# Kernel optimization log

Measured on AMD Instinct MI355X. Metric: run time of the kernel, lower is better.

Reference implementation:

```python
import jax, jax.numpy as jnp
import numpy as np

N_NODES = 10000
N_EDGES = 50000
N_GRAPHS = 64
NODE_DIM = 32
EDGE_DIM = 16
HID = 64
EDGE_HID = 128
OUT_DIM = 1
T_STEPS = 3       # message-passing rounds
S2S_STEPS = 6     # Set2Set processing steps


def setup_inputs() -> dict:
    key = jax.random.key(0)
    ks = jax.random.split(key, 24)
    def w(k, shape, scale):
        return (jax.random.normal(k, shape, dtype=jnp.float32) * scale)
    inp = {}
    inp["node_features"] = jax.random.normal(ks[0], (N_NODES, NODE_DIM), dtype=jnp.float32)
    inp["edge_features"] = jax.random.normal(ks[1], (N_EDGES, EDGE_DIM), dtype=jnp.float32)
    inp["edge_index"] = jax.random.randint(ks[2], (2, N_EDGES), 0, N_NODES, dtype=jnp.int32)
    # sorted, fully-covering graph assignment (nodes of each graph are contiguous)
    inp["batch_indices"] = ((jnp.arange(N_NODES) * N_GRAPHS) // N_NODES).astype(jnp.int32)
    # input projection
    inp["W_proj"] = w(ks[3], (NODE_DIM, HID), 1.0 / np.sqrt(NODE_DIM))
    inp["b_proj"] = jnp.zeros((HID,), jnp.float32)
    # edge network MLP: edge_dim -> edge_hid -> hid*hid
    inp["W_e1"] = w(ks[4], (EDGE_DIM, EDGE_HID), 1.0 / np.sqrt(EDGE_DIM))
    inp["b_e1"] = jnp.zeros((EDGE_HID,), jnp.float32)
    inp["W_e2"] = w(ks[5], (EDGE_HID, HID * HID), 0.01)
    inp["b_e2"] = jnp.zeros((HID * HID,), jnp.float32)
    # GRU cell (torch layout: 3*hid rows = r,z,n)
    inp["W_gih"] = w(ks[6], (3 * HID, HID), 1.0 / np.sqrt(HID))
    inp["W_ghh"] = w(ks[7], (3 * HID, HID), 1.0 / np.sqrt(HID))
    inp["b_gih"] = jnp.zeros((3 * HID,), jnp.float32)
    inp["b_ghh"] = jnp.zeros((3 * HID,), jnp.float32)
    # LSTM cell (torch layout: 4*hid rows = i,f,g,o), input 2*hid
    inp["W_lih"] = w(ks[8], (4 * HID, 2 * HID), 1.0 / np.sqrt(HID))
    inp["W_lhh"] = w(ks[9], (4 * HID, HID), 1.0 / np.sqrt(HID))
    inp["b_lih"] = jnp.zeros((4 * HID,), jnp.float32)
    inp["b_lhh"] = jnp.zeros((4 * HID,), jnp.float32)
    # readout MLP: 2*hid -> hid -> out
    inp["W_m1"] = w(ks[10], (2 * HID, HID), 1.0 / np.sqrt(2 * HID))
    inp["b_m1"] = jnp.zeros((HID,), jnp.float32)
    inp["W_m2"] = w(ks[11], (HID, OUT_DIM), 1.0 / np.sqrt(HID))
    inp["b_m2"] = jnp.zeros((OUT_DIM,), jnp.float32)
    return inp


def _scatter_softmax(e, idx, n_seg):
    mx = jax.ops.segment_max(e, idx, num_segments=n_seg)
    ex = jnp.exp(e - mx[idx])
    s = jax.ops.segment_sum(ex, idx, num_segments=n_seg)
    return ex / (s[idx] + 1e-16)


def _mpnn_forward(node_features, edge_features, edge_index, batch_indices,
                  W_proj, b_proj, W_e1, b_e1, W_e2, b_e2,
                  W_gih, W_ghh, b_gih, b_ghh,
                  W_lih, W_lhh, b_lih, b_lhh,
                  W_m1, b_m1, W_m2, b_m2):
    n_nodes = node_features.shape[0]
    dst = edge_index[0]  # receiving node v
    src = edge_index[1]  # sending node w

    # input projection
    h = node_features @ W_proj + b_proj                       # (N, H)

    # edge network: per-edge transformation matrix A(e_vw) (depends only on edge feats)
    A = jax.nn.relu(edge_features @ W_e1 + b_e1) @ W_e2 + b_e2
    A = A.reshape(-1, HID, HID)                               # (E, H, H)

    # T rounds: gather senders, per-edge bmm, scatter-add to receivers, GRU update
    for _ in range(T_STEPS):
        msgs = jnp.einsum('eij,ej->ei', A, h[src])            # (E, H)
        m = jax.ops.segment_sum(msgs, dst, num_segments=n_nodes)
        gx = m @ W_gih.T + b_gih                              # (N, 3H)
        gh = h @ W_ghh.T + b_ghh
        xr, xz, xn = jnp.split(gx, 3, axis=-1)
        hr, hz, hn = jnp.split(gh, 3, axis=-1)
        r = jax.nn.sigmoid(xr + hr)
        z = jax.nn.sigmoid(xz + hz)
        n = jnp.tanh(xn + r * hn)
        h = (1.0 - z) * n + z * h

    # Set2Set readout
    hs = jnp.zeros((N_GRAPHS, HID), h.dtype)
    cs = jnp.zeros((N_GRAPHS, HID), h.dtype)
    rs = jnp.zeros((N_GRAPHS, HID), h.dtype)
    for _ in range(S2S_STEPS):
        q = hs[batch_indices]                                 # (N, H)
        e = jnp.sum(h * q, axis=-1)                           # (N,)
        a = _scatter_softmax(e, batch_indices, N_GRAPHS)
        rs = jax.ops.segment_sum(a[:, None] * h, batch_indices, num_segments=N_GRAPHS)
        x = jnp.concatenate([hs, rs], axis=-1)                # (G, 2H)
        gates = x @ W_lih.T + b_lih + hs @ W_lhh.T + b_lhh    # (G, 4H)
        i, f, g, o = jnp.split(gates, 4, axis=-1)
        cs = jax.nn.sigmoid(f) * cs + jax.nn.sigmoid(i) * jnp.tanh(g)
        hs = jax.nn.sigmoid(o) * jnp.tanh(cs)
    ge = jnp.concatenate([hs, rs], axis=-1)                   # (G, 2H)
    return jax.nn.relu(ge @ W_m1 + b_m1) @ W_m2 + b_m2        # (G, out)


def reference(node_features, edge_features, edge_index, batch_indices,
              W_proj, b_proj, W_e1, b_e1, W_e2, b_e2,
              W_gih, W_ghh, b_gih, b_ghh,
              W_lih, W_lhh, b_lih, b_lhh,
              W_m1, b_m1, W_m2, b_m2):
    return _mpnn_forward(node_features, edge_features, edge_index, batch_indices,
                         W_proj, b_proj, W_e1, b_e1, W_e2, b_e2,
                         W_gih, W_ghh, b_gih, b_ghh,
                         W_lih, W_lhh, b_lih, b_lhh,
                         W_m1, b_m1, W_m2, b_m2)
```

## Files before the change

kernel.cpp:

```cpp
#include <hip/hip_runtime.h>

#define N_NODES   10000
#define N_EDGES   50000
#define N_GRAPHS  64
#define NODE_DIM  32
#define EDGE_DIM  16
#define HID       64
#define EHID      128
#define T_STEPS   3
#define S2S_STEPS 6

typedef _Float16 half_t;
typedef _Float16 f16x8 __attribute__((ext_vector_type(8)));
typedef float    f32x4 __attribute__((ext_vector_type(4)));

__device__ __forceinline__ float sigf(float x){ return 1.0f/(1.0f + expf(-x)); }

__global__ void k_zero(float* p, int n){
  int i = blockIdx.x*256 + threadIdx.x;
  if (i < n) p[i] = 0.0f;
}

__global__ void k_proj(const float* __restrict__ nf, const float* __restrict__ Wp,
                       const float* __restrict__ bp, float* __restrict__ h){
  int idx = blockIdx.x*256 + threadIdx.x;
  if (idx >= N_NODES*HID) return;
  int n = idx >> 6;
  int c = idx & 63;
  float acc = bp[c];
  const float* row = nf + (size_t)n*NODE_DIM;
  for (int j = 0; j < NODE_DIM; ++j)
    acc = fmaf(row[j], Wp[j*HID + c], acc);
  h[idx] = acc;
}

__global__ void k_tw2(const float* __restrict__ W2, float* __restrict__ Mm){
  int idx = blockIdx.x*256 + threadIdx.x;
  if (idx >= 64*8192) return;
  int j = idx >> 13; int o = idx & 8191; int k = o >> 6; int i = o & 63;
  Mm[idx] = W2[(size_t)k*4096 + i*64 + j];
}

__global__ void k_w2bt(const float* __restrict__ W2, half_t* __restrict__ BT){
  int idx = blockIdx.x*256 + threadIdx.x;
  if (idx >= 512*2*64*8) return;
  int j    = idx & 7;
  int lane = (idx >> 3) & 63;
  int tk   = (idx >> 9) & 1;
  int tn   = idx >> 10;
  int k = tk*32 + ((lane >> 4) << 3) + j;
  int o = tn*16 + (lane & 15);
  BT[idx] = (half_t)W2[(size_t)(o >> 6)*4096 + (o & 63)*64 + k];
}

__global__ void k_h2a(const float* __restrict__ h, half_t* __restrict__ AT){
  int idx = blockIdx.x*256 + threadIdx.x;
  if (idx >= 625*2*64*8) return;
  int j    = idx & 7;
  int lane = (idx >> 3) & 63;
  int tk   = (idx >> 9) & 1;
  int tm   = idx >> 10;
  int mrow = tm*16 + (lane & 15);
  int k    = tk*32 + ((lane >> 4) << 3) + j;
  AT[idx] = (half_t)h[(size_t)mrow*64 + k];
}

__global__ void k_twg(const float* __restrict__ Wg, const float* __restrict__ Wh,
                      float* __restrict__ WgT, float* __restrict__ WhT){
  int idx = blockIdx.x*256 + threadIdx.x;
  if (idx >= 192*64) return;
  int row = idx >> 6;
  int j   = idx & 63;
  WgT[j*192 + row] = Wg[(size_t)row*64 + j];
  WhT[j*192 + row] = Wh[(size_t)row*64 + j];
}

__global__ void k_ehid(const float* __restrict__ ef, const float* __restrict__ W1,
                       const float* __restrict__ b1, float* __restrict__ Hid){
  int idx = blockIdx.x*256 + threadIdx.x;
  if (idx >= N_EDGES*EHID) return;
  int e = idx >> 7, c = idx & 127;
  float acc = b1[c];
  const float* er = ef + (size_t)e*EDGE_DIM;
  for (int j = 0; j < EDGE_DIM; ++j)
    acc = fmaf(er[j], W1[j*EHID + c], acc);
  Hid[idx] = fmaxf(acc, 0.0f);
}

__global__ void k_bh(const float* __restrict__ h, const float* __restrict__ be2,
                     float* __restrict__ bh){
  int idx = blockIdx.x*256 + threadIdx.x;
  if (idx >= N_NODES*HID) return;
  int n = idx >> 6, i = idx & 63;
  float acc = 0.0f;
  const float* row = be2 + (size_t)i*64;
  const float* hr  = h + (size_t)n*64;
  for (int j = 0; j < 64; ++j)
    acc = fmaf(row[j], hr[j], acc);
  bh[idx] = acc;
}

__global__ void k_hist(const int* __restrict__ ei, int* __restrict__ deg){
  int e = blockIdx.x*256 + threadIdx.x;
  if (e >= N_EDGES) return;
  atomicAdd(&deg[ei[N_EDGES + e]], 1);
}

__global__ void k_scan(const int* __restrict__ deg, int* __restrict__ rowptr,
                       int* __restrict__ cursor){
  __shared__ int part[256];
  int t = threadIdx.x;
  int base = t*40;
  int s = 0;
  for (int i = 0; i < 40; ++i){
    int idx = base + i;
    if (idx < N_NODES) s += deg[idx];
  }
  part[t] = s;
  __syncthreads();
  for (int off = 1; off < 256; off <<= 1){
    int v = (t >= off) ? part[t - off] : 0;
    __syncthreads();
    part[t] += v;
    __syncthreads();
  }
  int run = (t > 0) ? part[t - 1] : 0;
  for (int i = 0; i < 40; ++i){
    int idx = base + i;
    if (idx < N_NODES){
      rowptr[idx] = run;
      cursor[idx] = run;
      run += deg[idx];
    }
  }
  if (t == 255) rowptr[N_NODES] = run;
}

__global__ void k_scatter(const int* __restrict__ ei, int* __restrict__ cursor,
                          int* __restrict__ csr){
  int e = blockIdx.x*256 + threadIdx.x;
  if (e >= N_EDGES) return;
  int src = ei[N_EDGES + e];
  int pos = atomicAdd(&cursor[src], 1);
  csr[pos] = e;
}

__global__ void k_cgemm_mfma(const half_t* __restrict__ AT,
                             const half_t* __restrict__ BT,
                             half_t* __restrict__ C){
  __shared__ half_t tile[4][16][64];
  int wv   = threadIdx.x >> 6;
  int lane = threadIdx.x & 63;
  int tm = blockIdx.x*4 + wv;
  bool active = (tm < 625);
  if (!active) tm = 624;
  const f16x8* Ab = (const f16x8*)AT + (size_t)tm*128;
  f16x8 a0 = Ab[lane];
  f16x8 a1 = Ab[64 + lane];
  int tn0 = blockIdx.y*4;
  f32x4 acc[4];
  #pragma unroll
  for (int s = 0; s < 4; ++s){ acc[s][0]=0.f; acc[s][1]=0.f; acc[s][2]=0.f; acc[s][3]=0.f; }
  #pragma unroll
  for (int s = 0; s < 4; ++s){
    const f16x8* Bb = (const f16x8*)BT + (size_t)(tn0 + s)*128;
    f16x8 b0 = Bb[lane];
    f16x8 b1 = Bb[64 + lane];
    acc[s] = __builtin_amdgcn_mfma_f32_16x16x32_f16(a0, b0, acc[s], 0, 0, 0);
    acc[s] = __builtin_amdgcn_mfma_f32_16x16x32_f16(a1, b1, acc[s], 0, 0, 0);
  }
  int quad = lane >> 4;
  int colb = lane & 15;
  #pragma unroll
  for (int s = 0; s < 4; ++s)
    #pragma unroll
    for (int r = 0; r < 4; ++r)
      tile[wv][quad*4 + r][s*16 + colb] = (half_t)acc[s][r];
  __syncthreads();
  if (active){
    int row = lane >> 3;
    int c0  = (lane & 7)*8;
    size_t base = (size_t)tm*16*8192 + (size_t)tn0*16;
    f16x8 v0 = *(const f16x8*)&tile[wv][row][c0];
    f16x8 v1 = *(const f16x8*)&tile[wv][row + 8][c0];
    *(f16x8*)&C[base + (size_t)row*8192 + c0]       = v0;
    *(f16x8*)&C[base + (size_t)(row + 8)*8192 + c0] = v1;
  }
}

__global__ void k_cgemm(const float* __restrict__ h, const float* __restrict__ Mm,
                        half_t* __restrict__ C, int lo, int hi){
  __shared__ float hs[16][64];
  int n0 = lo + blockIdx.x*16;
  int o0 = blockIdx.y*256 + threadIdx.x;
  for (int idx = threadIdx.x; idx < 16*64; idx += 256){
    int nn = idx >> 6, j = idx & 63;
    int node = n0 + nn;
    hs[nn][j] = (node < hi) ? h[(size_t)node*64 + j] : 0.0f;
  }
  __syncthreads();
  float acc0[16], acc1[16];
  #pragma unroll
  for (int nn = 0; nn < 16; ++nn){ acc0[nn] = 0.0f; acc1[nn] = 0.0f; }
  for (int j4 = 0; j4 < 16; ++j4){
    const float* M0 = Mm + (size_t)(j4*4)*8192;
    float a0 = M0[o0],            b0 = M0[o0 + 4096];
    float a1 = M0[8192 + o0],     b1 = M0[8192 + o0 + 4096];
    float a2 = M0[2*8192 + o0],   b2 = M0[2*8192 + o0 + 4096];
    float a3 = M0[3*8192 + o0],   b3 = M0[3*8192 + o0 + 4096];
    #pragma unroll
    for (int nn = 0; nn < 16; ++nn){
      float4 hv = *(const float4*)&hs[nn][j4*4];
      acc0[nn] = fmaf(hv.x, a0, acc0[nn]);
      acc1[nn] = fmaf(hv.x, b0, acc1[nn]);
      acc0[nn] = fmaf(hv.y, a1, acc0[nn]);
      acc1[nn] = fmaf(hv.y, b1, acc1[nn]);
      acc0[nn] = fmaf(hv.z, a2, acc0[nn]);
      acc1[nn] = fmaf(hv.z, b2, acc1[nn]);
      acc0[nn] = fmaf(hv.w, a3, acc0[nn]);
      acc1[nn] = fmaf(hv.w, b3, acc1[nn]);
    }
  }
  #pragma unroll
  for (int nn = 0; nn < 16; ++nn){
    int node = n0 + nn;
    if (node < hi){
      half_t* Cr = C + (size_t)(node - lo)*8192;
      Cr[o0]        = (half_t)acc0[nn];
      Cr[o0 + 4096] = (half_t)acc1[nn];
    }
  }
}

__global__ void MPNN_55705725829535_kernel(const int* __restrict__ rowptr,
                                           const int* __restrict__ csr,
                                           const int* __restrict__ ei,
                                           const float* __restrict__ Hid,
                                           const half_t* __restrict__ C,
                                           const float* __restrict__ bh,
                                           float* __restrict__ m, int lo, int hi){
  __shared__ float hidL[4][8][128];
  int wave = threadIdx.x >> 6;
  int lane = threadIdx.x & 63;
  int s = lo + blockIdx.x*4 + wave;
  if (s >= hi) return;
  int beg = rowptr[s];
  int endp = rowptr[s + 1];
  if (beg == endp) return;
  float bhv = bh[(size_t)s*64 + lane];
  const half_t* Cb = C + (size_t)(s - lo)*8192 + lane;
  float (*hl)[128] = hidL[wave];
  for (int gbeg = beg; gbeg < endp; gbeg += 8){
    int gn = endp - gbeg; if (gn > 8) gn = 8;
    int dsts[8];
    int e0 = csr[gbeg];
    #pragma unroll
    for (int j = 0; j < 8; ++j){
      int e = (j < gn) ? csr[gbeg + j] : e0;
      dsts[j] = ei[e];
      hl[j][lane]      = Hid[(size_t)e*128 + lane];
      hl[j][lane + 64] = Hid[(size_t)e*128 + 64 + lane];
    }
    float acc[8];
    #pragma unroll
    for (int j = 0; j < 8; ++j) acc[j] = 0.0f;
    #pragma unroll 4
    for (int k = 0; k < 128; ++k){
      float c = (float)Cb[k*64];
      #pragma unroll
      for (int j = 0; j < 8; ++j)
        acc[j] = fmaf(hl[j][k], c, acc[j]);
    }
    for (int j = 0; j < gn; ++j)
      atomicAdd(&m[(size_t)dsts[j]*64 + lane], acc[j] + bhv);
  }
}

__global__ void k_msg_fb(const int* __restrict__ ei, const float* __restrict__ ef,
                         const float* __restrict__ W1, const float* __restrict__ b1,
                         const float* __restrict__ W2, const float* __restrict__ be2,
                         const float* __restrict__ h, float* __restrict__ m){
  __shared__ float HidL[EHID];
  __shared__ __align__(16) float hsL[HID];
  int e = blockIdx.x;
  int t = threadIdx.x;
  int src = ei[N_EDGES + e];
  int dst = ei[e];
  {
    float a0 = b1[t];
    float a1 = b1[t + 64];
    const float* er = ef + (size_t)e*EDGE_DIM;
    for (int j = 0; j < EDGE_DIM; ++j){
      float ev = er[j];
      a0 = fmaf(ev, W1[j*EHID + t],      a0);
      a1 = fmaf(ev, W1[j*EHID + t + 64], a1);
    }
    HidL[t]      = fmaxf(a0, 0.0f);
    HidL[t + 64] = fmaxf(a1, 0.0f);
    hsL[t] = h[(size_t)src*64 + t];
  }
  __syncthreads();
  float acc = 0.0f;
  for (int k = 0; k < EHID; ++k){
    float s = HidL[k];
    if (s != 0.0f){
      const float* w = W2 + (size_t)k*4096 + t*64;
      float partial = 0.0f;
      for (int j = 0; j < 64; ++j)
        partial = fmaf(hsL[j], w[j], partial);
      acc = fmaf(s, partial, acc);
    }
  }
  {
    const float* w = be2 + (size_t)t*64;
    for (int j = 0; j < 64; ++j)
      acc = fmaf(hsL[j], w[j], acc);
  }
  atomicAdd(&m[(size_t)dst*64 + t], acc);
}

__global__ void k_gru(float* __restrict__ h, const float* __restrict__ m,
                      const float* __restrict__ WgT, const float* __restrict__ WhT,
                      const float* __restrict__ bg, const float* __restrict__ bhb){
  __shared__ float mld[16][64];
  __shared__ float hld[16][64];
  int t  = threadIdx.x;
  int i  = t & 63;
  int wv = t >> 6;
  int n0 = blockIdx.x*16;
  for (int idx = t; idx < 16*64; idx += 256){
    int nn = idx >> 6, j = idx & 63;
    int node = n0 + nn;
    mld[nn][j] = m[(size_t)node*64 + j];
    hld[nn][j] = h[(size_t)node*64 + j];
  }
  __syncthreads();
  float xr[4], xz[4], xn[4], hr[4], hz[4], hn[4];
  #pragma unroll
  for (int c = 0; c < 4; ++c){
    xr[c] = bg[i];  xz[c] = bg[64 + i];  xn[c] = bg[128 + i];
    hr[c] = bhb[i]; hz[c] = bhb[64 + i]; hn[c] = bhb[128 + i];
  }
  for (int j = 0; j < 64; ++j){
    const float* wg = WgT + j*192;
    const float* wh = WhT + j*192;
    float wgr = wg[i], wgz = wg[64 + i], wgn = wg[128 + i];
    float whr = wh[i], whz = wh[64 + i], whn = wh[128 + i];
    #pragma unroll
    for (int c = 0; c < 4; ++c){
      int nn = wv*4 + c;
      float mj = mld[nn][j];
      float hj = hld[nn][j];
      xr[c] = fmaf(mj, wgr, xr[c]);
      xz[c] = fmaf(mj, wgz, xz[c]);
      xn[c] = fmaf(mj, wgn, xn[c]);
      hr[c] = fmaf(hj, whr, hr[c]);
      hz[c] = fmaf(hj, whz, hz[c]);
      hn[c] = fmaf(hj, whn, hn[c]);
    }
  }
  #pragma unroll
  for (int c = 0; c < 4; ++c){
    int nn = wv*4 + c;
    float r  = sigf(xr[c] + hr[c]);
    float z  = sigf(xz[c] + hz[c]);
    float nv = tanhf(xn[c] + r*hn[c]);
    h[(size_t)(n0 + nn)*64 + i] = (1.0f - z)*nv + z*hld[nn][i];
  }
}

__global__ void k_s2s(const float* __restrict__ h,
                      const float* __restrict__ Wli, const float* __restrict__ Wlh,
                      const float* __restrict__ bli, const float* __restrict__ blh,
                      const float* __restrict__ Wm1, const float* __restrict__ bm1,
                      const float* __restrict__ Wm2, const float* __restrict__ bm2,
                      float* __restrict__ out){
  __shared__ float hc[157*65];
  __shared__ float ea[160];
  __shared__ float x[192];
  __shared__ float gpart[512];
  __shared__ float rsp[8][64];
  __shared__ float wredA[8];
  __shared__ float wredB[8];
  __shared__ float hsb[64];
  __shared__ float csb[64];
  __shared__ float rsb[64];
  int g = blockIdx.x;
  int t = threadIdx.x;
  int lane = t & 63;
  int wv   = t >> 6;
  int start = (g*N_NODES + 63) >> 6;
  int end   = ((g + 1)*N_NODES + 63) >> 6;
  int cnt = end - start;
  const float* hg = h + (size_t)start*64;
  for (int idx = t; idx < cnt*64; idx += 512)
    hc[(idx >> 6)*65 + (idx & 63)] = hg[idx];
  if (t < 64){ hsb[t] = 0.0f; csb[t] = 0.0f; rsb[t] = 0.0f; }
  __syncthreads();
  for (int step = 0; step < S2S_STEPS; ++step){
    float ev = -1e30f;
    if (t < cnt){
      float a = 0.0f;
      const float* hr = &hc[t*65];
      for (int i = 0; i < 64; ++i) a = fmaf(hr[i], hsb[i], a);
      ev = a;
    }
    float v = ev;
    for (int o = 32; o > 0; o >>= 1) v = fmaxf(v, __shfl_xor(v, o));
    if (lane == 0) wredA[wv] = v;
    __syncthreads();
    float mx = wredA[0];
    #pragma unroll
    for (int i = 1; i < 8; ++i) mx = fmaxf(mx, wredA[i]);
    float ex = (t < cnt) ? expf(ev - mx) : 0.0f;
    float sv = ex;
    for (int o = 32; o > 0; o >>= 1) sv += __shfl_xor(sv, o);
    if (lane == 0) wredB[wv] = sv;
    __syncthreads();
    float ssum = 0.0f;
    #pragma unroll
    for (int i = 0; i < 8; ++i) ssum += wredB[i];
    if (t < cnt) ea[t] = ex / (ssum + 1e-16f);
    __syncthreads();
    {
      int n0 = wv*20;
      int n1 = n0 + 20; if (n1 > cnt) n1 = cnt;
      float r = 0.0f;
      for (int n = n0; n < n1; ++n)
        r = fmaf(ea[n], hc[n*65 + lane], r);
      rsp[wv][lane] = r;
    }
    __syncthreads();
    if (t < 64){
      float r = rsp[0][t] + rsp[1][t] + rsp[2][t] + rsp[3][t]
              + rsp[4][t] + rsp[5][t] + rsp[6][t] + rsp[7][t];
      rsb[t] = r;
      x[t]        = hsb[t];
      x[64 + t]   = r;
      x[128 + t]  = hsb[t];
    }
    __syncthreads();
    {
      int gate = t & 255;
      int half = t >> 8;
      float gl = 0.0f;
      if (half == 0){
        const float* wr = Wli + (size_t)gate*128;
        for (int jj = 0; jj < 96; ++jj) gl = fmaf(x[jj], wr[jj], gl);
      } else {
        const float* wr = Wli + (size_t)gate*128;
        for (int jj = 96; jj < 128; ++jj) gl = fmaf(x[jj], wr[jj], gl);
        const float* wh = Wlh + (size_t)gate*64;
        for (int jj = 0; jj < 64; ++jj) gl = fmaf(x[128 + jj], wh[jj], gl);
      }
      gpart[t] = gl;
    }
    __syncthreads();
    if (t < 64){
      float iv = sigf (gpart[t]       + gpart[t + 256]       + bli[t]       + blh[t]);
      float fv = sigf (gpart[64 + t]  + gpart[64 + t + 256]  + bli[64 + t]  + blh[64 + t]);
      float gv = tanhf(gpart[128 + t] + gpart[128 + t + 256] + bli[128 + t] + blh[128 + t]);
      float ov = sigf (gpart[192 + t] + gpart[192 + t + 256] + bli[192 + t] + blh[192 + t]);
      float c  = fv*csb[t] + iv*gv;
      csb[t] = c;
      hsb[t] = ov*tanhf(c);
    }
    __syncthreads();
  }
  float rv = 0.0f;
  if (t < 64){
    float v = bm1[t];
    for (int j = 0; j < 64; ++j) v = fmaf(hsb[j], Wm1[(size_t)j*64 + t],        v);
    for (int j = 0; j < 64; ++j) v = fmaf(rsb[j], Wm1[(size_t)(64 + j)*64 + t], v);
    v = fmaxf(v, 0.0f);
    rv = v * Wm2[t];
  }
  for (int o = 32; o > 0; o >>= 1) rv += __shfl_xor(rv, o);
  if (lane == 0) wredA[wv] = rv;
  __syncthreads();
  if (t == 0) out[g] = wredA[0] + wredA[1] + wredA[2] + wredA[3]
                     + wredA[4] + wredA[5] + wredA[6] + wredA[7] + bm2[0];
}

extern "C" void kernel_launch(void* const* d_in, const int* in_sizes, int n_in,
                              void* d_out, int out_size, void* d_ws, size_t ws_size,
                              hipStream_t stream){
  (void)in_sizes; (void)n_in; (void)out_size;

  const float* nf  = (const float*)d_in[0];
  const float* ef  = (const float*)d_in[1];
  const int*   ei  = (const int*)d_in[2];
  const float* Wp  = (const float*)d_in[4];
  const float* bp  = (const float*)d_in[5];
  const float* We1 = (const float*)d_in[6];
  const float* be1 = (const float*)d_in[7];
  const float* We2 = (const float*)d_in[8];
  const float* be2 = (const float*)d_in[9];
  const float* Wg  = (const float*)d_in[10];
  const float* Wh  = (const float*)d_in[11];
  const float* bg  = (const float*)d_in[12];
  const float* bhb = (const float*)d_in[13];
  const float* Wli = (const float*)d_in[14];
  const float* Wlh = (const float*)d_in[15];
  const float* bli = (const float*)d_in[16];
  const float* blh = (const float*)d_in[17];
  const float* Wm1 = (const float*)d_in[18];
  const float* bm1 = (const float*)d_in[19];
  const float* Wm2 = (const float*)d_in[20];
  const float* bm2 = (const float*)d_in[21];

  float* out = (float*)d_out;
  float* ws  = (float*)d_ws;

  float* h    = ws;
  float* m    = ws + 640000;
  float* bh   = ws + 1280000;
  float* Mm   = ws + 1920000;
  float* WgT  = ws + 2444288;
  float* WhT  = ws + 2456576;
  float* Hid  = ws + 2468864;
  int*   deg    = (int*)(ws + 8868864);
  int*   rowptr = deg + 10000;
  int*   cursor = rowptr + 10001;
  int*   csr    = cursor + 10000;
  half_t* AT  = (half_t*)(ws + 8948880);
  half_t* BT  = (half_t*)(ws + 9268880);
  const size_t C_OFF = 9531024;
  half_t* C   = (half_t*)(ws + C_OFF);

  long long c_halves = ((long long)ws_size - (long long)C_OFF*4) / 2;
  int NC = (c_halves > 0) ? (int)(c_halves / 8192) : 0;
  if (NC > N_NODES) NC = N_NODES;
  int use_c_path = (NC >= 512);
  int use_mfma   = (NC >= N_NODES);

  k_proj<<<(N_NODES*HID + 255)/256, 256, 0, stream>>>(nf, Wp, bp, h);

  if (use_c_path){
    k_twg <<<(192*64 + 255)/256, 256, 0, stream>>>(Wg, Wh, WgT, WhT);
    k_ehid<<<(N_EDGES*EHID + 255)/256, 256, 0, stream>>>(ef, We1, be1, Hid);
    k_zero<<<(10000 + 255)/256, 256, 0, stream>>>((float*)deg, 10000);
    k_hist<<<(N_EDGES + 255)/256, 256, 0, stream>>>(ei, deg);
    k_scan<<<1, 256, 0, stream>>>(deg, rowptr, cursor);
    k_scatter<<<(N_EDGES + 255)/256, 256, 0, stream>>>(ei, cursor, csr);
    if (use_mfma){
      k_w2bt<<<(512*2*64*8 + 255)/256, 256, 0, stream>>>(We2, BT);
      for (int step = 0; step < T_STEPS; ++step){
        k_zero<<<(N_NODES*HID + 255)/256, 256, 0, stream>>>(m, N_NODES*HID);
        k_bh<<<(N_NODES*HID + 255)/256, 256, 0, stream>>>(h, be2, bh);
        k_h2a<<<(625*2*64*8 + 255)/256, 256, 0, stream>>>(h, AT);
        dim3 grid(157, 128);
        k_cgemm_mfma<<<grid, 256, 0, stream>>>(AT, BT, C);
        MPNN_55705725829535_kernel<<<(N_NODES + 3)/4, 256, 0, stream>>>(
            rowptr, csr, ei, Hid, C, bh, m, 0, N_NODES);
        k_gru<<<625, 256, 0, stream>>>(h, m, WgT, WhT, bg, bhb);
      }
    } else {
      k_tw2<<<(64*8192)/256, 256, 0, stream>>>(We2, Mm);
      for (int step = 0; step < T_STEPS; ++step){
        k_zero<<<(N_NODES*HID + 255)/256, 256, 0, stream>>>(m, N_NODES*HID);
        k_bh<<<(N_NODES*HID + 255)/256, 256, 0, stream>>>(h, be2, bh);
        for (int lo = 0; lo < N_NODES; lo += NC){
          int hi = (lo + NC < N_NODES) ? lo + NC : N_NODES;
          int cnt = hi - lo;
          dim3 grid((cnt + 15)/16, 16);
          k_cgemm<<<grid, 256, 0, stream>>>(h, Mm, C, lo, hi);
          MPNN_55705725829535_kernel<<<(cnt + 3)/4, 256, 0, stream>>>(
              rowptr, csr, ei, Hid, C, bh, m, lo, hi);
        }
        k_gru<<<625, 256, 0, stream>>>(h, m, WgT, WhT, bg, bhb);
      }
    }
  } else {
    k_twg <<<(192*64 + 255)/256, 256, 0, stream>>>(Wg, Wh, WgT, WhT);
    for (int step = 0; step < T_STEPS; ++step){
      k_zero<<<(N_NODES*HID + 255)/256, 256, 0, stream>>>(m, N_NODES*HID);
      k_msg_fb<<<N_EDGES, 64, 0, stream>>>(ei, ef, We1, be1, We2, be2, h, m);
      k_gru<<<625, 256, 0, stream>>>(h, m, WgT, WhT, bg, bhb);
    }
  }
  k_s2s<<<N_GRAPHS, 512, 0, stream>>>(h, Wli, Wlh, bli, blh,
                                      Wm1, bm1, Wm2, bm2, out);
}
```

Before: 653.0 us.

## Use MFMA for per-edge message contraction with fp16 edge hidden features

The per-source message kernel now batches up to 16 outgoing edges and computes their messages with 16x16x32 fp16 MFMA against the node's precomputed C slab, which is held in registers. Edge hidden activations are stored as fp16 so they can be fed straight in as MFMA operands. The C-producing GEMM is retiled so each block covers one 16-node tile and a quarter of K, writing C in a fragment-friendly layout. This targets the scalar FMA and LDS traffic of the old message loop, at the cost of lower precision in Hid and more atomics issued per lane.

```diff
diff --git a/kernel.cpp b/kernel.cpp
--- a/kernel.cpp
+++ b/kernel.cpp
@@ -87,6 +87,18 @@
   Hid[idx] = fmaxf(acc, 0.0f);
 }
 
+__global__ void k_ehid16(const float* __restrict__ ef, const float* __restrict__ W1,
+                         const float* __restrict__ b1, half_t* __restrict__ Hid16){
+  int idx = blockIdx.x*256 + threadIdx.x;
+  if (idx >= N_EDGES*EHID) return;
+  int e = idx >> 7, c = idx & 127;
+  float acc = b1[c];
+  const float* er = ef + (size_t)e*EDGE_DIM;
+  for (int j = 0; j < EDGE_DIM; ++j)
+    acc = fmaf(er[j], W1[j*EHID + c], acc);
+  Hid16[idx] = (half_t)fmaxf(acc, 0.0f);
+}
+
 __global__ void k_bh(const float* __restrict__ h, const float* __restrict__ be2,
                      float* __restrict__ bh){
   int idx = blockIdx.x*256 + threadIdx.x;
@@ -148,43 +160,44 @@
 __global__ void k_cgemm_mfma(const half_t* __restrict__ AT,
                              const half_t* __restrict__ BT,
                              half_t* __restrict__ C){
-  __shared__ half_t tile[4][16][64];
   int wv   = threadIdx.x >> 6;
   int lane = threadIdx.x & 63;
-  int tm = blockIdx.x*4 + wv;
-  bool active = (tm < 625);
-  if (!active) tm = 624;
+  int tm   = blockIdx.x;
+  int kt   = blockIdx.y;
   const f16x8* Ab = (const f16x8*)AT + (size_t)tm*128;
   f16x8 a0 = Ab[lane];
   f16x8 a1 = Ab[64 + lane];
-  int tn0 = blockIdx.y*4;
-  f32x4 acc[4];
-  #pragma unroll
-  for (int s = 0; s < 4; ++s){ acc[s][0]=0.f; acc[s][1]=0.f; acc[s][2]=0.f; acc[s][3]=0.f; }
-  #pragma unroll
-  for (int s = 0; s < 4; ++s){
-    const f16x8* Bb = (const f16x8*)BT + (size_t)(tn0 + s)*128;
-    f16x8 b0 = Bb[lane];
-    f16x8 b1 = Bb[64 + lane];
-    acc[s] = __builtin_amdgcn_mfma_f32_16x16x32_f16(a0, b0, acc[s], 0, 0, 0);
-    acc[s] = __builtin_amdgcn_mfma_f32_16x16x32_f16(a1, b1, acc[s], 0, 0, 0);
+  f32x4 acc[4][8];
+  #pragma unroll
+  for (int is = 0; is < 4; ++is)
+    #pragma unroll
+    for (int jj = 0; jj < 8; ++jj){
+      acc[is][jj][0]=0.f; acc[is][jj][1]=0.f; acc[is][jj][2]=0.f; acc[is][jj][3]=0.f;
+    }
+  #pragma unroll
+  for (int jj = 0; jj < 8; ++jj){
+    int ke = kt*32 + wv*8 + jj;
+    const f16x8* Bb = (const f16x8*)BT + (size_t)(ke*4)*128 + lane;
+    #pragma unroll
+    for (int is = 0; is < 4; ++is){
+      f16x8 b0 = Bb[is*128];
+      f16x8 b1 = Bb[is*128 + 64];
+      acc[is][jj] = __builtin_amdgcn_mfma_f32_16x16x32_f16(a0, b0, acc[is][jj], 0, 0, 0);
+      acc[is][jj] = __builtin_amdgcn_mfma_f32_16x16x32_f16(a1, b1, acc[is][jj], 0, 0, 0);
+    }
   }
   int quad = lane >> 4;
   int colb = lane & 15;
   #pragma unroll
-  for (int s = 0; s < 4; ++s)
-    #pragma unroll
-    for (int r = 0; r < 4; ++r)
-      tile[wv][quad*4 + r][s*16 + colb] = (half_t)acc[s][r];
-  __syncthreads();
-  if (active){
-    int row = lane >> 3;
-    int c0  = (lane & 7)*8;
-    size_t base = (size_t)tm*16*8192 + (size_t)tn0*16;
-    f16x8 v0 = *(const f16x8*)&tile[wv][row][c0];
-    f16x8 v1 = *(const f16x8*)&tile[wv][row + 8][c0];
-    *(f16x8*)&C[base + (size_t)row*8192 + c0]       = v0;
-    *(f16x8*)&C[base + (size_t)(row + 8)*8192 + c0] = v1;
+  for (int r = 0; r < 4; ++r){
+    int n = tm*16 + quad*4 + r;
+    #pragma unroll
+    for (int is = 0; is < 4; ++is){
+      f16x8 v;
+      #pragma unroll
+      for (int jj = 0; jj < 8; ++jj) v[jj] = (half_t)acc[is][jj][r];
+      *(f16x8*)&C[(size_t)n*8192 + kt*2048 + is*512 + (size_t)(wv*16 + colb)*8] = v;
+    }
   }
 }
 
@@ -235,10 +248,79 @@
 __global__ void MPNN_55705725829535_kernel(const int* __restrict__ rowptr,
                                            const int* __restrict__ csr,
                                            const int* __restrict__ ei,
-                                           const float* __restrict__ Hid,
+                                           const half_t* __restrict__ Hid16,
                                            const half_t* __restrict__ C,
                                            const float* __restrict__ bh,
-                                           float* __restrict__ m, int lo, int hi){
+                                           float* __restrict__ m){
+  __shared__ int dstL[4][16];
+  int wave = threadIdx.x >> 6;
+  int lane = threadIdx.x & 63;
+  int s = blockIdx.x*4 + wave;
+  if (s >= N_NODES) return;
+  int beg  = rowptr[s];
+  int endp = rowptr[s + 1];
+  if (beg == endp) return;
+  int quad = lane >> 4;
+  int colb = lane & 15;
+  const f16x8* Cb = (const f16x8*)(C + (size_t)s*8192) + lane;
+  f16x8 B[4][4];
+  #pragma unroll
+  for (int kt = 0; kt < 4; ++kt)
+    #pragma unroll
+    for (int is = 0; is < 4; ++is)
+      B[kt][is] = Cb[kt*256 + is*64];
+  float bhc[4];
+  #pragma unroll
+  for (int is = 0; is < 4; ++is)
+    bhc[is] = bh[(size_t)s*64 + is*16 + colb];
+  for (int gbeg = beg; gbeg < endp; gbeg += 16){
+    int gn = endp - gbeg; if (gn > 16) gn = 16;
+    if (lane < 16)
+      dstL[wave][lane] = (lane < gn) ? ei[csr[gbeg + lane]] : -1;
+    f16x8 A[4];
+    if (colb < gn){
+      int e = csr[gbeg + colb];
+      const f16x8* Hb = (const f16x8*)(Hid16 + (size_t)e*128) + quad;
+      #pragma unroll
+      for (int kt = 0; kt < 4; ++kt)
+        A[kt] = Hb[kt*4];
+    } else {
+      #pragma unroll
+      for (int kt = 0; kt < 4; ++kt)
+        #pragma unroll
+        for (int q = 0; q < 8; ++q) A[kt][q] = (half_t)0;
+    }
+    f32x4 acc[4];
+    #pragma unroll
+    for (int is = 0; is < 4; ++is){
+      acc[is][0]=0.f; acc[is][1]=0.f; acc[is][2]=0.f; acc[is][3]=0.f;
+    }
+    #pragma unroll
+    for (int kt = 0; kt < 4; ++kt)
+      #pragma unroll
+      for (int is = 0; is < 4; ++is)
+        acc[is] = __builtin_amdgcn_mfma_f32_16x16x32_f16(A[kt], B[kt][is], acc[is], 0, 0, 0);
+    #pragma unroll
+    for (int r = 0; r < 4; ++r){
+      int jrow = quad*4 + r;
+      if (jrow < gn){
+        int d = dstL[wave][jrow];
+        float* mr = m + (size_t)d*64 + colb;
+        #pragma unroll
+        for (int is = 0; is < 4; ++is)
+          atomicAdd(mr + is*16, acc[is][r] + bhc[is]);
+      }
+    }
+  }
+}
+
+__global__ void k_msg_csr(const int* __restrict__ rowptr,
+                          const int* __restrict__ csr,
+                          const int* __restrict__ ei,
+                          const float* __restrict__ Hid,
+                          const half_t* __restrict__ C,
+                          const float* __restrict__ bh,
+                          float* __restrict__ m, int lo, int hi){
   __shared__ float hidL[4][8][128];
   int wave = threadIdx.x >> 6;
   int lane = threadIdx.x & 63;
@@ -519,6 +601,7 @@
   float* WgT  = ws + 2444288;
   float* WhT  = ws + 2456576;
   float* Hid  = ws + 2468864;
+  half_t* Hid16 = (half_t*)Hid;
   int*   deg    = (int*)(ws + 8868864);
   int*   rowptr = deg + 10000;
   int*   cursor = rowptr + 10001;
@@ -538,24 +621,25 @@
 
   if (use_c_path){
     k_twg <<<(192*64 + 255)/256, 256, 0, stream>>>(Wg, Wh, WgT, WhT);
-    k_ehid<<<(N_EDGES*EHID + 255)/256, 256, 0, stream>>>(ef, We1, be1, Hid);
     k_zero<<<(10000 + 255)/256, 256, 0, stream>>>((float*)deg, 10000);
     k_hist<<<(N_EDGES + 255)/256, 256, 0, stream>>>(ei, deg);
     k_scan<<<1, 256, 0, stream>>>(deg, rowptr, cursor);
     k_scatter<<<(N_EDGES + 255)/256, 256, 0, stream>>>(ei, cursor, csr);
     if (use_mfma){
+      k_ehid16<<<(N_EDGES*EHID + 255)/256, 256, 0, stream>>>(ef, We1, be1, Hid16);
       k_w2bt<<<(512*2*64*8 + 255)/256, 256, 0, stream>>>(We2, BT);
       for (int step = 0; step < T_STEPS; ++step){
         k_zero<<<(N_NODES*HID + 255)/256, 256, 0, stream>>>(m, N_NODES*HID);
         k_bh<<<(N_NODES*HID + 255)/256, 256, 0, stream>>>(h, be2, bh);
         k_h2a<<<(625*2*64*8 + 255)/256, 256, 0, stream>>>(h, AT);
-        dim3 grid(157, 128);
+        dim3 grid(625, 4);
         k_cgemm_mfma<<<grid, 256, 0, stream>>>(AT, BT, C);
         MPNN_55705725829535_kernel<<<(N_NODES + 3)/4, 256, 0, stream>>>(
-            rowptr, csr, ei, Hid, C, bh, m, 0, N_NODES);
+            rowptr, csr, ei, Hid16, C, bh, m);
         k_gru<<<625, 256, 0, stream>>>(h, m, WgT, WhT, bg, bhb);
       }
     } else {
+      k_ehid<<<(N_EDGES*EHID + 255)/256, 256, 0, stream>>>(ef, We1, be1, Hid);
       k_tw2<<<(64*8192)/256, 256, 0, stream>>>(We2, Mm);
       for (int step = 0; step < T_STEPS; ++step){
         k_zero<<<(N_NODES*HID + 255)/256, 256, 0, stream>>>(m, N_NODES*HID);
@@ -565,7 +649,7 @@
           int cnt = hi - lo;
           dim3 grid((cnt + 15)/16, 16);
           k_cgemm<<<grid, 256, 0, stream>>>(h, Mm, C, lo, hi);
-          MPNN_55705725829535_kernel<<<(cnt + 3)/4, 256, 0, stream>>>(
+          k_msg_csr<<<(cnt + 3)/4, 256, 0, stream>>>(
               rowptr, csr, ei, Hid, C, bh, m, lo, hi);
         }
         k_gru<<<625, 256, 0, stream>>>(h, m, WgT, WhT, bg, bhb);
```

Measured after the change: 613.8 us. 1.06x faster.
